# Optimization experiments

Hardware: AMD Instinct MI355X
Metric: run time of the kernel (lower is better)

The kernel has to match this reference:

```python
import jax, jax.numpy as jnp
import numpy as np

UNIF_T = 2.0
EPS = 1e-12  # matches F.normalize default eps


def _l2norm(a):
    return a / jnp.maximum(jnp.linalg.norm(a, axis=-1, keepdims=True), EPS)


def setup_inputs() -> dict:
    key = jax.random.key(0)
    k1, k2, k3, k4 = jax.random.split(key, 4)
    n, d = 2048, 512
    Q, K = 3, 8192
    n_classes = 16
    x = jax.random.normal(k1, (n, d), dtype=jnp.float32)
    q_data = jax.random.normal(k2, (Q, K, d), dtype=jnp.float32)
    targets = jax.random.randint(k3, (n,), 0, n_classes, dtype=jnp.int64)
    q_targets = jax.random.randint(k4, (Q, K), 0, n_classes, dtype=jnp.int64)
    return {"x": x, "q_data": q_data, "targets": targets, "q_targets": q_targets, "order": 1}


def reference(x, q_data, targets, q_targets, order):
    # x: [n, d], q_data: [Q, K, d], targets: [n], q_targets: [Q, K]
    Q, K, _ = q_data.shape
    xn = _l2norm(x)
    qn = _l2norm(q_data)
    sim = jnp.einsum('nd,qkd->qnk', xn, qn)      # [Q, n, K]
    e = jnp.exp(-UNIF_T * (2.0 - 2.0 * sim))     # [Q, n, K]
    # mask[i, j] = targets[i] == q_targets[order, j]; masked entries of the
    # `order` queue are excluded from that row's mean.
    mask = targets[:, None] == q_targets[order][None, :]   # [n, K] bool
    total = e.sum(axis=(0, 2))                              # [n]
    masked_sum = jnp.where(mask, e[order], 0.0).sum(axis=1) # [n]
    count = (Q * K - mask.sum(axis=1)).astype(e.dtype)      # [n]
    loss = jnp.mean(jnp.log((total - masked_sum) / count))
    return loss
```

## Files before the change

### kernel.cpp

```cpp
#include <hip/hip_runtime.h>
#include <hip/hip_bf16.h>
#include <cstdint>
#include <cstddef>

#define N_ROWS 2048
#define DIM    512
#define QN     3
#define KQ     8192
#define NCOL   (QN * KQ)
#define NCLASS 16

#define BM 128
#define BN 128
#define BK 128
#define NBLK (NCOL / BN)

typedef __attribute__((ext_vector_type(4))) float f32x4;

__global__ __launch_bounds__(256) void norm_cast_kernel(
    const float* __restrict__ x, const float* __restrict__ q,
    unsigned char* __restrict__ xb, unsigned char* __restrict__ qb,
    float* __restrict__ out) {
    if (blockIdx.x == 0 && threadIdx.x == 0) out[0] = 0.f;
    int row = blockIdx.x * 4 + (threadIdx.x >> 6);
    int lane = threadIdx.x & 63;
    const float* src;
    unsigned char* dst;
    if (row < N_ROWS) {
        src = x + (size_t)row * DIM;
        dst = xb + (size_t)row * DIM;
    } else {
        src = q + (size_t)(row - N_ROWS) * DIM;
        dst = qb + (size_t)(row - N_ROWS) * DIM;
    }
    float4 v0 = ((const float4*)src)[lane * 2];
    float4 v1 = ((const float4*)src)[lane * 2 + 1];
    float ss = v0.x*v0.x + v0.y*v0.y + v0.z*v0.z + v0.w*v0.w
             + v1.x*v1.x + v1.y*v1.y + v1.z*v1.z + v1.w*v1.w;
    #pragma unroll
    for (int off = 1; off < 64; off <<= 1)
        ss += __shfl_xor(ss, off, 64);
    float inv = 16.0f / fmaxf(sqrtf(ss), 1e-12f);
    int w0 = __builtin_amdgcn_cvt_pk_fp8_f32(v0.x * inv, v0.y * inv, 0,  false);
    w0     = __builtin_amdgcn_cvt_pk_fp8_f32(v0.z * inv, v0.w * inv, w0, true);
    int w1 = __builtin_amdgcn_cvt_pk_fp8_f32(v1.x * inv, v1.y * inv, 0,  false);
    w1     = __builtin_amdgcn_cvt_pk_fp8_f32(v1.z * inv, v1.w * inv, w1, true);
    uint2 o; o.x = (unsigned)w0; o.y = (unsigned)w1;
    int r3 = (row >> 3) & 1;
    *(uint2*)(dst + ((lane * 8) ^ (r3 << 3))) = o;
}

__global__ __launch_bounds__(256) void gemm_epilogue_kernel(
    const unsigned char* __restrict__ Xb,
    const unsigned char* __restrict__ Qb,
    const int* __restrict__ targets,
    const int* __restrict__ q_targets,
    const int* __restrict__ order_p,
    float* __restrict__ P) {

    __shared__ unsigned char As[BM * BK];
    __shared__ unsigned char Bs[BN * BK];

    const int tid  = threadIdx.x;
    const int lane = tid & 63;
    const int wave = tid >> 6;
    const int wm = wave >> 1, wn = wave & 1;
    const int quad = lane >> 4;
    const int l15  = lane & 15;
    const int l7   = l15 & 7;
    const int l3   = (l15 >> 3) & 1;

    const int b    = blockIdx.x;
    const int xcd  = b & 7;
    const int g    = b >> 3;
    const int colb = (g >> 4) * 8 + xcd;
    const int rowb = g & 15;
    const int m0 = rowb * BM;
    const int n0 = colb * BN;

    f32x4 acc[4][4];
    #pragma unroll
    for (int i = 0; i < 4; i++)
        #pragma unroll
        for (int j = 0; j < 4; j++)
            acc[i][j] = (f32x4){0.f, 0.f, 0.f, 0.f};

    const int stR = (lane >> 3);
    const int stC = ((lane & 7) ^ stR) * 16;

    for (int k0 = 0; k0 < DIM; k0 += BK) {
        #pragma unroll
        for (int j = 0; j < 4; j++) {
            int chunk = wave * 4 + j;
            int R = chunk * 8 + stR;
            const unsigned char* ga = Xb + (size_t)(m0 + R) * DIM + k0 + stC;
            const unsigned char* gb = Qb + (size_t)(n0 + R) * DIM + k0 + stC;
            __builtin_amdgcn_global_load_lds(
                (const __attribute__((address_space(1))) unsigned int*)ga,
                (__attribute__((address_space(3))) unsigned int*)&As[chunk * 1024 + lane * 16],
                16, 0, 0);
            __builtin_amdgcn_global_load_lds(
                (const __attribute__((address_space(1))) unsigned int*)gb,
                (__attribute__((address_space(3))) unsigned int*)&Bs[chunk * 1024 + lane * 16],
                16, 0, 0);
        }
        __syncthreads();

        #pragma unroll
        for (int ks = 0; ks < BK; ks += 32) {
            const int sw = ((((ks >> 4) + (quad >> 1)) ^ l7) << 4)
                         + (((quad & 1) ^ l3) << 3);
            long a[4], bb[4];
            #pragma unroll
            for (int mt = 0; mt < 4; mt++)
                a[mt] = *(const long*)&As[(wm * 64 + mt * 16 + l15) * BK + sw];
            #pragma unroll
            for (int nt = 0; nt < 4; nt++)
                bb[nt] = *(const long*)&Bs[(wn * 64 + nt * 16 + l15) * BK + sw];
            #pragma unroll
            for (int mt = 0; mt < 4; mt++)
                #pragma unroll
                for (int nt = 0; nt < 4; nt++)
                    acc[mt][nt] = __builtin_amdgcn_mfma_f32_16x16x32_fp8_fp8(
                        a[mt], bb[nt], acc[mt][nt], 0, 0, 0);
        }
        __syncthreads();
    }

    const int ord  = order_p[0];
    const int qIdx = colb / (KQ / BN);
    const bool isOrd = (qIdx == ord);
    const int kbase = n0 - qIdx * KQ;

    int qtv[4] = {0, 0, 0, 0};
    if (isOrd) {
        #pragma unroll
        for (int nt = 0; nt < 4; nt++)
            qtv[nt] = q_targets[ord * KQ + kbase + wn * 64 + nt * 16 + l15];
    }

    float* red = (float*)As;

    #pragma unroll
    for (int mt = 0; mt < 4; mt++) {
        int rowl = wm * 64 + mt * 16 + quad * 4;
        int tg[4] = {0, 0, 0, 0};
        if (isOrd) {
            #pragma unroll
            for (int reg = 0; reg < 4; reg++) tg[reg] = targets[m0 + rowl + reg];
        }
        #pragma unroll
        for (int reg = 0; reg < 4; reg++) {
            float s = 0.f;
            #pragma unroll
            for (int nt = 0; nt < 4; nt++) {
                float v256 = acc[mt][nt][reg];
                float e = __expf(v256 * 0.015625f - 4.0f);
                if (isOrd && tg[reg] == qtv[nt]) e = 0.f;
                s += e;
            }
            s += __shfl_xor(s, 1, 64);
            s += __shfl_xor(s, 2, 64);
            s += __shfl_xor(s, 4, 64);
            s += __shfl_xor(s, 8, 64);
            if (l15 == 0)
                red[wn * 128 + rowl + reg] = s;
        }
    }
    __syncthreads();
    if (tid < 128)
        P[(size_t)colb * N_ROWS + m0 + tid] = red[tid] + red[128 + tid];
}

__global__ __launch_bounds__(256) void reduce_kernel(
    const float* __restrict__ P,
    const int* __restrict__ targets,
    const int* __restrict__ q_targets,
    const int* __restrict__ order_p,
    float* __restrict__ out) {
    __shared__ int hist[NCLASS];
    __shared__ float partial[4];
    int tid = threadIdx.x;
    int wave = tid >> 6, lane = tid & 63;
    if (tid < NCLASS) hist[tid] = 0;
    __syncthreads();
    int ord = order_p[0];

    int local[NCLASS];
    #pragma unroll
    for (int c = 0; c < NCLASS; c++) local[c] = 0;
    for (int i = tid; i < KQ; i += 256) {
        int v = q_targets[ord * KQ + i];
        #pragma unroll
        for (int c = 0; c < NCLASS; c++)
            local[c] += __popcll(__ballot(v == c));
    }
    if (lane == 0) {
        #pragma unroll
        for (int c = 0; c < NCLASS; c++)
            atomicAdd(&hist[c], local[c]);
    }
    __syncthreads();

    int r = blockIdx.x * 256 + tid;
    float total = 0.f;
    #pragma unroll 8
    for (int nb = 0; nb < NBLK; nb++)
        total += P[(size_t)nb * N_ROWS + r];
    float cnt = (float)(QN * KQ - hist[targets[r]]);
    float v = logf(total / cnt);

    #pragma unroll
    for (int off = 1; off < 64; off <<= 1)
        v += __shfl_xor(v, off, 64);
    if (lane == 0) partial[wave] = v;
    __syncthreads();
    if (tid == 0)
        atomicAdd(out, (partial[0] + partial[1] + partial[2] + partial[3])
                       * (1.0f / (float)N_ROWS));
}

extern "C" void kernel_launch(void* const* d_in, const int* in_sizes, int n_in,
                              void* d_out, int out_size, void* d_ws, size_t ws_size,
                              hipStream_t stream) {
    const float* x         = (const float*)d_in[0];
    const float* q         = (const float*)d_in[1];
    const int*   targets   = (const int*)d_in[2];
    const int*   q_targets = (const int*)d_in[3];
    const int*   order     = (const int*)d_in[4];
    float* out = (float*)d_out;

    char* ws = (char*)d_ws;
    float* P = (float*)ws;
    unsigned char* Xb = (unsigned char*)(ws + (size_t)NBLK * N_ROWS * 4);
    unsigned char* Qb = Xb + (size_t)N_ROWS * DIM;

    norm_cast_kernel<<<(N_ROWS + NCOL) / 4, 256, 0, stream>>>(x, q, Xb, Qb, out);

    gemm_epilogue_kernel<<<NBLK * (N_ROWS / BM), 256, 0, stream>>>(
        Xb, Qb, targets, q_targets, order, P);

    reduce_kernel<<<N_ROWS / 256, 256, 0, stream>>>(P, targets, q_targets, order, out);
}
```

Before: 164.4 us.

## Use gfx950 scaled 16x16x128 FP8 MFMA with 16-byte LDS fragment loads

Replaces the four 16x16x32 FP8 MFMAs per K-slab with a single mfma_scale 16x16x128 f8f6f4 instruction using unit scales (0x7F exponent). The LDS fragment read pattern becomes two 16-byte swizzled loads per tile in place of 8-byte loads, and the fp8 write swizzle in the normalize kernel is removed to match. The goal is to cut MFMA instruction count, use the higher-throughput gfx950 FP8 path and widen LDS reads. It depends on the K-to-lane mapping of the new instruction matching the swizzle, and it raises register pressure.

```diff
diff --git a/kernel.cpp b/kernel.cpp
--- a/kernel.cpp
+++ b/kernel.cpp
@@ -16,6 +16,8 @@
 #define NBLK (NCOL / BN)
 
 typedef __attribute__((ext_vector_type(4))) float f32x4;
+typedef __attribute__((ext_vector_type(4))) int   iv4;
+typedef __attribute__((ext_vector_type(8))) int   iv8;
 
 __global__ __launch_bounds__(256) void norm_cast_kernel(
     const float* __restrict__ x, const float* __restrict__ q,
@@ -46,8 +48,7 @@
     int w1 = __builtin_amdgcn_cvt_pk_fp8_f32(v1.x * inv, v1.y * inv, 0,  false);
     w1     = __builtin_amdgcn_cvt_pk_fp8_f32(v1.z * inv, v1.w * inv, w1, true);
     uint2 o; o.x = (unsigned)w0; o.y = (unsigned)w1;
-    int r3 = (row >> 3) & 1;
-    *(uint2*)(dst + ((lane * 8) ^ (r3 << 3))) = o;
+    *(uint2*)(dst + lane * 8) = o;
 }
 
 __global__ __launch_bounds__(256) void gemm_epilogue_kernel(
@@ -68,7 +69,6 @@
     const int quad = lane >> 4;
     const int l15  = lane & 15;
     const int l7   = l15 & 7;
-    const int l3   = (l15 >> 3) & 1;
 
     const int b    = blockIdx.x;
     const int xcd  = b & 7;
@@ -87,6 +87,9 @@
 
     const int stR = (lane >> 3);
     const int stC = ((lane & 7) ^ stR) * 16;
+
+    const int slotLo = (((quad << 1)    ) ^ l7) << 4;
+    const int slotHi = (((quad << 1) | 1) ^ l7) << 4;
 
     for (int k0 = 0; k0 < DIM; k0 += BK) {
         #pragma unroll
@@ -106,24 +109,30 @@
         }
         __syncthreads();
 
-        #pragma unroll
-        for (int ks = 0; ks < BK; ks += 32) {
-            const int sw = ((((ks >> 4) + (quad >> 1)) ^ l7) << 4)
-                         + (((quad & 1) ^ l3) << 3);
-            long a[4], bb[4];
-            #pragma unroll
-            for (int mt = 0; mt < 4; mt++)
-                a[mt] = *(const long*)&As[(wm * 64 + mt * 16 + l15) * BK + sw];
+        iv8 a[4], bb[4];
+        #pragma unroll
+        for (int mt = 0; mt < 4; mt++) {
+            const unsigned char* base = &As[(wm * 64 + mt * 16 + l15) * BK];
+            iv4 lo = *(const iv4*)(base + slotLo);
+            iv4 hi = *(const iv4*)(base + slotHi);
+            a[mt] = __builtin_shufflevector(lo, hi, 0, 1, 2, 3, 4, 5, 6, 7);
+        }
+        #pragma unroll
+        for (int nt = 0; nt < 4; nt++) {
+            const unsigned char* base = &Bs[(wn * 64 + nt * 16 + l15) * BK];
+            iv4 lo = *(const iv4*)(base + slotLo);
+            iv4 hi = *(const iv4*)(base + slotHi);
+            bb[nt] = __builtin_shufflevector(lo, hi, 0, 1, 2, 3, 4, 5, 6, 7);
+        }
+        #pragma unroll
+        for (int mt = 0; mt < 4; mt++)
             #pragma unroll
             for (int nt = 0; nt < 4; nt++)
-                bb[nt] = *(const long*)&Bs[(wn * 64 + nt * 16 + l15) * BK + sw];
-            #pragma unroll
-            for (int mt = 0; mt < 4; mt++)
-                #pragma unroll
-                for (int nt = 0; nt < 4; nt++)
-                    acc[mt][nt] = __builtin_amdgcn_mfma_f32_16x16x32_fp8_fp8(
-                        a[mt], bb[nt], acc[mt][nt], 0, 0, 0);
-        }
+                acc[mt][nt] = __builtin_amdgcn_mfma_scale_f32_16x16x128_f8f6f4(
+                    a[mt], bb[nt], acc[mt][nt],
+                    0, 0,
+                    0, 0x7F7F7F7F,
+                    0, 0x7F7F7F7F);
         __syncthreads();
     }
 
```

After: 207.2 us. 26.0% more time.
